# Kernel tuning notes

Hardware: AMD Instinct MI355X
Metric: run time of the kernel (lower is better)

The kernel has to match this reference:

```python
import jax, jax.numpy as jnp
import numpy as np

B, N, D = 8, 2048, 3
HIDDEN = (64, 128, 256)
LATENT = 128


def _layernorm(x, scale, bias, eps=1e-6):
    mu = jnp.mean(x, axis=-1, keepdims=True)
    var = jnp.mean((x - mu) ** 2, axis=-1, keepdims=True)
    return (x - mu) / jnp.sqrt(var + eps) * scale + bias


def setup_inputs() -> dict:
    key = jax.random.key(0)
    ks = jax.random.split(key, 8)
    inp = {
        "x": jax.random.normal(ks[0], (B, N, D), dtype=jnp.float32),
        "mask": jnp.ones((B, N), dtype=jnp.float32),
    }
    in_d = D
    for i, d in enumerate(HIDDEN):
        inp[f"W{i}"] = (jax.random.normal(ks[1 + i], (in_d, d), dtype=jnp.float32)
                        / np.float32(np.sqrt(in_d)))
        inp[f"b{i}"] = jnp.zeros((d,), dtype=jnp.float32)
        inp[f"g{i}"] = jnp.ones((d,), dtype=jnp.float32)
        inp[f"be{i}"] = jnp.zeros((d,), dtype=jnp.float32)
        in_d = d
    inp["Wz"] = (jax.random.normal(ks[5], (in_d, LATENT), dtype=jnp.float32)
                 / np.float32(np.sqrt(in_d)))
    inp["bz"] = jnp.zeros((LATENT,), dtype=jnp.float32)
    return inp


def reference(x, mask, W0, b0, g0, be0, W1, b1, g1, be1, W2, b2, g2, be2, Wz, bz):
    m = mask[..., None]                                   # (B, N, 1)
    count = jnp.sum(m, axis=1)                            # (B, 1)
    centroid = jnp.sum(x * m, axis=1, keepdims=True) / jnp.maximum(count, 1.0)[:, None, :]
    xc = x - centroid                                     # (B, N, D)

    # Pairwise squared distances; attention depends only on coordinates,
    # so it is identical for every layer -> compute once.
    diff = xc[:, :, None, :] - xc[:, None, :, :]          # (B, N, N, D)
    dist = jnp.sum(diff * diff, axis=-1)                  # (B, N, N)
    attn = jax.nn.softmax(-dist, axis=-1)                 # (B, N, N)

    h = xc
    for W, b, g, be in ((W0, b0, g0, be0), (W1, b1, g1, be1), (W2, b2, g2, be2)):
        h_agg = jnp.einsum('bij,bjd->bid', attn, h)       # weighted aggregation
        h = h_agg @ W + b
        h = _layernorm(h, g, be)
        h = jax.nn.swish(h)

    # Invariant readout: masked mean pool then Dense(latent)
    global_feat = jnp.sum(h * m, axis=1) / jnp.maximum(count, 1.0)
    z = global_feat @ Wz + bz                             # (B, latent)
    return z
```

## Files before the change

kernel.cpp:

```cpp
#include <hip/hip_runtime.h>
#include <hip/hip_bf16.h>

#define BATCH 8
#define NPTS 2048
#define LATENT 128

typedef __attribute__((ext_vector_type(8))) short short8;
typedef __attribute__((ext_vector_type(4))) float f32x4;

__device__ __forceinline__ ushort f2bf(float f) {
  unsigned int b = __float_as_uint(f);
  b += 0x7FFF + ((b >> 16) & 1);
  return (ushort)(b >> 16);
}
__device__ __forceinline__ float bf2f(ushort u) {
  return __uint_as_float(((unsigned int)u) << 16);
}
__device__ __forceinline__ unsigned int pkbf(float a, float b) {
  __hip_bfloat162 h = __float22bfloat162_rn(make_float2(a, b));
  return *(unsigned int*)&h;
}

typedef unsigned int __attribute__((address_space(1))) gas_uint;
typedef unsigned int __attribute__((address_space(3))) las_uint;
__device__ __forceinline__ void gl_lds16(const void* g, void* l) {
  __builtin_amdgcn_global_load_lds((const gas_uint*)g, (las_uint*)l, 16, 0, 0);
}

#define L2E 1.4426950408889634f
#define SC2 1.6986436f

__device__ __forceinline__ void wtrans_tile(const float* __restrict__ W,
    ushort* __restrict__ WT, int K, int N, int n0, int k0, int tid) {
  __shared__ ushort s[64][72];
  for (int i = tid; i < 64 * 64; i += 256) {
    const int kl = i >> 6, nl = i & 63;
    s[kl][nl] = f2bf(W[(size_t)(k0 + kl) * N + n0 + nl]);
  }
  __syncthreads();
  for (int i = tid; i < 64 * 64; i += 256) {
    const int nl = i >> 6, kl = i & 63;
    WT[(size_t)(n0 + nl) * K + k0 + kl] = s[kl][nl];
  }
}

__global__ __launch_bounds__(256) void setup_kernel(const float* __restrict__ x,
    const float* __restrict__ mask, float4* __restrict__ pnt,
    const float* __restrict__ W1, ushort* __restrict__ WT1,
    const float* __restrict__ W2, ushort* __restrict__ WT2,
    const float* __restrict__ Wz, ushort* __restrict__ WzT) {
  const int bid = blockIdx.x;
  const int tid = threadIdx.x;
  if (bid >= 8) {
    if (bid < 10) wtrans_tile(W1, WT1, 64, 128, (bid - 8) * 64, 0, tid);
    else if (bid < 18) {
      const int idx = bid - 10;
      wtrans_tile(W2, WT2, 128, 256, (idx & 3) * 64, (idx >> 2) * 64, tid);
    } else {
      const int idx = bid - 18;
      wtrans_tile(Wz, WzT, 256, 128, (idx & 1) * 64, (idx >> 1) * 64, tid);
    }
    return;
  }
  const int b = bid;
  const float* xb = x + (size_t)b * NPTS * 3;
  const float* mb = mask + (size_t)b * NPTS;
  float s0 = 0.f, s1 = 0.f, s2 = 0.f, c = 0.f;
  for (int n = tid; n < NPTS; n += 256) {
    float m = mb[n];
    s0 += xb[n * 3 + 0] * m;
    s1 += xb[n * 3 + 1] * m;
    s2 += xb[n * 3 + 2] * m;
    c += m;
  }
  __shared__ float red[4][256];
  red[0][tid] = s0; red[1][tid] = s1; red[2][tid] = s2; red[3][tid] = c;
  __syncthreads();
  for (int off = 128; off > 0; off >>= 1) {
    if (tid < off) {
      red[0][tid] += red[0][tid + off];
      red[1][tid] += red[1][tid + off];
      red[2][tid] += red[2][tid + off];
      red[3][tid] += red[3][tid + off];
    }
    __syncthreads();
  }
  const float cnt = fmaxf(red[3][0], 1.0f);
  const float c0 = red[0][0] / cnt, c1 = red[1][0] / cnt, c2 = red[2][0] / cnt;
  float4* pb = pnt + (size_t)b * NPTS;
  for (int n = tid; n < NPTS; n += 256) {
    const float a0 = xb[n * 3 + 0] - c0;
    const float a1 = xb[n * 3 + 1] - c1;
    const float a2 = xb[n * 3 + 2] - c2;
    pb[n] = make_float4(a0 * SC2, a1 * SC2, a2 * SC2,
                        -(a0 * a0 + a1 * a1 + a2 * a2) * L2E);
  }
}

__global__ __launch_bounds__(512) void layer0_kernel(
    const float4* __restrict__ pnt, const float* __restrict__ W,
    const float* __restrict__ bias, const float* __restrict__ g,
    const float* __restrict__ be, ushort* __restrict__ hout) {
  const int b = blockIdx.y;
  const int i0 = blockIdx.x * 64;
  const int tid = threadIdx.x;
  const int il = tid & 63, part = tid >> 6;
  const float4* pb = pnt + (size_t)b * NPTS;
  const float4 pi = pb[i0 + il];
  float a0 = 0.f, a1 = 0.f, a2 = 0.f, dn = 0.f;
#pragma unroll 8
  for (int j = part * 256; j < part * 256 + 256; j++) {
    const float4 pj = pb[j];
    float arg = pi.w + pj.w;
    arg = fmaf(pi.x, pj.x, arg);
    arg = fmaf(pi.y, pj.y, arg);
    arg = fmaf(pi.z, pj.z, arg);
    const float w = __builtin_amdgcn_exp2f(arg);
    a0 = fmaf(w, pj.x, a0);
    a1 = fmaf(w, pj.y, a1);
    a2 = fmaf(w, pj.z, a2);
    dn += w;
  }
  __shared__ float4 sred[8][64];
  __shared__ float srow[64 * 3];
  __shared__ ushort lt[64][64];
  sred[part][il] = make_float4(a0, a1, a2, dn);
  __syncthreads();
  if (tid < 64) {
    float A0 = 0.f, A1 = 0.f, A2 = 0.f, DN = 0.f;
#pragma unroll
    for (int p = 0; p < 8; p++) {
      const float4 r = sred[p][tid];
      A0 += r.x; A1 += r.y; A2 += r.z; DN += r.w;
    }
    const float inv = 1.0f / (DN * SC2);
    srow[tid * 3 + 0] = A0 * inv;
    srow[tid * 3 + 1] = A1 * inv;
    srow[tid * 3 + 2] = A2 * inv;
  }
  __syncthreads();
  const int wv = tid >> 6, lane = tid & 63;
  const float w0c = W[lane], w1c = W[64 + lane], w2c = W[128 + lane];
  const float gv = g[lane], bev = be[lane], bv = bias[lane];
#pragma unroll
  for (int r = 0; r < 8; r++) {
    const int row = wv * 8 + r;
    float o = bv;
    o = fmaf(srow[row * 3 + 0], w0c, o);
    o = fmaf(srow[row * 3 + 1], w1c, o);
    o = fmaf(srow[row * 3 + 2], w2c, o);
    float m1 = o, m2 = o * o;
#pragma unroll
    for (int off = 32; off > 0; off >>= 1) {
      m1 += __shfl_xor(m1, off, 64);
      m2 += __shfl_xor(m2, off, 64);
    }
    const float mu = m1 / 64.f;
    const float rstd = rsqrtf(m2 / 64.f - mu * mu + 1e-6f);
    const float v = (o - mu) * rstd * gv + bev;
    const float act = v / (1.0f + __expf(-v));
    lt[row][lane] = f2bf(act);
  }
  __syncthreads();
  if (tid < 64) {
    ushort tmp[64];
#pragma unroll
    for (int r = 0; r < 64; r++) tmp[r] = lt[r][tid];
    ushort* dst = hout + ((size_t)b * 64 + tid) * NPTS + i0;
#pragma unroll
    for (int c = 0; c < 8; c++)
      *(uint4*)(dst + c * 8) = *(uint4*)&tmp[c * 8];
  }
}

template <int DIN, int DOUT, bool POOL>
__global__ __launch_bounds__(512, 2) void fused_v5(
    const float4* __restrict__ pnt, const ushort* __restrict__ hT,
    const ushort* __restrict__ WT, const float* __restrict__ bias,
    const float* __restrict__ g, const float* __restrict__ be,
    ushort* __restrict__ hout, const float* __restrict__ mask,
    float* __restrict__ partial) {
  constexpr int NT = DIN / 16;
  constexpr int HALF = NPTS / 2;
  constexpr int TILES = HALF / 64;
  constexpr int NCOL = DOUT / 32;
  constexpr int PS = DIN + 8;
  constexpr int PN = DIN + 4;
  constexpr int SHT_B = 2 * 2 * DIN * 64 * 2;
  constexpr int SPNT_B = 2 * 2 * 64 * 16;
  constexpr int LOOP_B = SHT_B + SPNT_B;
  constexpr int SNUM_B = 64 * PN * 4;
  constexpr int OFF_SROW = SNUM_B;
  constexpr int OFF_SDEN = OFF_SROW + 64 * PS * 2;
  constexpr int OFF_SINV = OFF_SDEN + 256;
  constexpr int OFF_SSTAT = OFF_SINV + 256;
  constexpr int EPI_B = OFF_SSTAT + 1024;
  constexpr int SMEM_B = LOOP_B > EPI_B ? LOOP_B : EPI_B;
  __shared__ __align__(16) char smem[SMEM_B];
  ushort* sht = (ushort*)smem;
  float4* spnt = (float4*)(smem + SHT_B);

  const int b = blockIdx.y;
  const int i0 = blockIdx.x * 64;
  const int tid = threadIdx.x;
  const int wv = tid >> 6, lane = tid & 63;
  const int h = (wv >> 1) & 1;
  const int u = wv & 1;
  const int rg = wv >> 2;
  const int m = lane & 15, q = lane >> 4;
  const float4* pb = pnt + (size_t)b * NPTS;
  const ushort* hb = hT + (size_t)b * DIN * NPTS;

  const float4 pi0 = pb[i0 + rg * 32 + m];
  const float4 pi1 = pb[i0 + rg * 32 + 16 + m];

  f32x4 acc0[NT], acc1[NT];
#pragma unroll
  for (int nt = 0; nt < NT; nt++)
#pragma unroll
    for (int e = 0; e < 4; e++) { acc0[nt][e] = 0.f; acc1[nt][e] = 0.f; }
  float dacc0 = 0.f, dacc1 = 0.f;

  constexpr int NCH = DIN / 32;
  const int srow8 = lane >> 3;
  const int scsrc = (lane & 7) ^ srow8;
  const int jsw = ((lane & 7) << 3) | (lane >> 3);

  auto stage = [&](int t, int bf) {
    const int jb = t * 64;
#pragma unroll
    for (int i = 0; i < NCH; i++) {
      const int idx = wv * NCH + i;
      const int h2 = idx / (DIN / 8);
      const int oct = idx % (DIN / 8);
      const int row = oct * 8 + srow8;
      gl_lds16(hb + (size_t)row * NPTS + h2 * HALF + jb + scsrc * 8,
               sht + ((size_t)(bf * 2 + h2) * DIN + oct * 8) * 64);
    }
    if (wv == 0) {
#pragma unroll
      for (int h2 = 0; h2 < 2; h2++)
        gl_lds16(pb + h2 * HALF + jb + jsw, spnt + (bf * 2 + h2) * 64);
    }
  };

  stage(0, 0);
  __syncthreads();
  for (int t = 0; t < TILES; t++) {
    const int bf = t & 1;
    if (t + 1 < TILES) stage(t + 1, bf ^ 1);
    unsigned int au0[4], au1[4];
#pragma unroll
    for (int p = 0; p < 4; p++) {
      float wp[4];
#pragma unroll
      for (int e = 0; e < 2; e++) {
        const int jj = 2 * p + e;
        const float4 pj = spnt[(bf * 2 + h) * 64 + ((jj << 3) | (u * 4 + q))];
        float a0 = pi0.w + pj.w;
        a0 = fmaf(pi0.x, pj.x, a0);
        a0 = fmaf(pi0.y, pj.y, a0);
        a0 = fmaf(pi0.z, pj.z, a0);
        float a1 = pi1.w + pj.w;
        a1 = fmaf(pi1.x, pj.x, a1);
        a1 = fmaf(pi1.y, pj.y, a1);
        a1 = fmaf(pi1.z, pj.z, a1);
        wp[e] = __builtin_amdgcn_exp2f(a0);
        wp[2 + e] = __builtin_amdgcn_exp2f(a1);
      }
      dacc0 += wp[0] + wp[1];
      dacc1 += wp[2] + wp[3];
      au0[p] = pkbf(wp[0], wp[1]);
      au1[p] = pkbf(wp[2], wp[3]);
    }
    const short8 af0 = *(short8*)au0;
    const short8 af1 = *(short8*)au1;
#pragma unroll
    for (int nt = 0; nt < NT; nt++) {
      const int d = nt * 16 + m;
      const short8 bfr = *(const short8*)
          &sht[((size_t)(bf * 2 + h) * DIN + d) * 64 + (((u * 4 + q) ^ (m & 7)) << 3)];
      acc0[nt] = __builtin_amdgcn_mfma_f32_16x16x32_bf16(af0, bfr, acc0[nt], 0, 0, 0);
      acc1[nt] = __builtin_amdgcn_mfma_f32_16x16x32_bf16(af1, bfr, acc1[nt], 0, 0, 0);
    }
    __syncthreads();
  }

  float* snum = (float*)smem;
  ushort* srow = (ushort*)(smem + OFF_SROW);
  float* sden = (float*)(smem + OFF_SDEN);
  float* sinv = (float*)(smem + OFF_SINV);
  float* sstat = (float*)(smem + OFF_SSTAT);

  dacc0 += __shfl_xor(dacc0, 16, 64);
  dacc0 += __shfl_xor(dacc0, 32, 64);
  dacc1 += __shfl_xor(dacc1, 16, 64);
  dacc1 += __shfl_xor(dacc1, 32, 64);
  const int quarter = wv & 3;
  for (int p = 0; p < 4; p++) {
    if (quarter == p) {
      if (p == 0) {
#pragma unroll
        for (int nt = 0; nt < NT; nt++)
#pragma unroll
          for (int r = 0; r < 4; r++) {
            snum[(rg * 32 + q * 4 + r) * PN + nt * 16 + m] = acc0[nt][r];
            snum[(rg * 32 + 16 + q * 4 + r) * PN + nt * 16 + m] = acc1[nt][r];
          }
        if (q == 0) {
          sden[rg * 32 + m] = dacc0;
          sden[rg * 32 + 16 + m] = dacc1;
        }
      } else {
#pragma unroll
        for (int nt = 0; nt < NT; nt++)
#pragma unroll
          for (int r = 0; r < 4; r++) {
            snum[(rg * 32 + q * 4 + r) * PN + nt * 16 + m] += acc0[nt][r];
            snum[(rg * 32 + 16 + q * 4 + r) * PN + nt * 16 + m] += acc1[nt][r];
          }
        if (q == 0) {
          sden[rg * 32 + m] += dacc0;
          sden[rg * 32 + 16 + m] += dacc1;
        }
      }
    }
    __syncthreads();
  }
  if (tid < 64) sinv[tid] = 1.0f / sden[tid];
  __syncthreads();
  for (int idx = tid; idx < 64 * (DIN / 2); idx += 512) {
    const int r = idx / (DIN / 2), c2 = idx % (DIN / 2);
    const float v0 = snum[r * PN + 2 * c2] * sinv[r];
    const float v1 = snum[r * PN + 2 * c2 + 1] * sinv[r];
    *(unsigned int*)&srow[r * PS + 2 * c2] = pkbf(v0, v1);
  }
  __syncthreads();

  const int rg2 = wv >> 1, ch = wv & 1;
  short8 afrag[DIN / 32];
#pragma unroll
  for (int kt = 0; kt < DIN / 32; kt++)
    afrag[kt] = *(const short8*)&srow[(rg2 * 16 + m) * PS + kt * 32 + q * 8];
  f32x4 oacc[NCOL];
#pragma unroll
  for (int c = 0; c < NCOL; c++)
#pragma unroll
    for (int e = 0; e < 4; e++) oacc[c][e] = 0.f;
#pragma unroll
  for (int c = 0; c < NCOL; c++) {
    const int n0 = (ch * NCOL + c) * 16;
#pragma unroll
    for (int kt = 0; kt < DIN / 32; kt++) {
      const short8 bfrag = *(const short8*)(WT + (size_t)(n0 + m) * DIN + kt * 32 + q * 8);
      oacc[c] = __builtin_amdgcn_mfma_f32_16x16x32_bf16(afrag[kt], bfrag, oacc[c], 0, 0, 0);
    }
  }

  float bcol[NCOL];
#pragma unroll
  for (int c = 0; c < NCOL; c++) bcol[c] = bias[(ch * NCOL + c) * 16 + m];
#pragma unroll
  for (int r = 0; r < 4; r++) {
    float m1 = 0.f, m2 = 0.f;
#pragma unroll
    for (int c = 0; c < NCOL; c++) {
      const float v = oacc[c][r] + bcol[c];
      m1 += v; m2 += v * v;
    }
#pragma unroll
    for (int off = 8; off > 0; off >>= 1) {
      m1 += __shfl_xor(m1, off, 64);
      m2 += __shfl_xor(m2, off, 64);
    }
    if (m == 0) {
      const int row = rg2 * 16 + q * 4 + r;
      sstat[(row * 2 + ch) * 2 + 0] = m1;
      sstat[(row * 2 + ch) * 2 + 1] = m2;
    }
  }
  __syncthreads();

  ushort* lt = (ushort*)smem;
  float* spl = (float*)smem;
  float pacc[NCOL];
  if (POOL) {
#pragma unroll
    for (int c = 0; c < NCOL; c++) pacc[c] = 0.f;
  }
#pragma unroll
  for (int r = 0; r < 4; r++) {
    const int row = rg2 * 16 + q * 4 + r;
    const float m1 = sstat[(row * 2 + 0) * 2 + 0] + sstat[(row * 2 + 1) * 2 + 0];
    const float m2 = sstat[(row * 2 + 0) * 2 + 1] + sstat[(row * 2 + 1) * 2 + 1];
    const float mu = m1 / DOUT;
    const float rstd = rsqrtf(m2 / DOUT - mu * mu + 1e-6f);
    float mval = 0.f;
    if (POOL) mval = mask[(size_t)b * NPTS + i0 + row];
#pragma unroll
    for (int c = 0; c < NCOL; c++) {
      const int dco = (ch * NCOL + c) * 16 + m;
      const float v = (oacc[c][r] + bcol[c] - mu) * rstd * g[dco] + be[dco];
      const float act = v / (1.0f + __expf(-v));
      if (POOL) pacc[c] = fmaf(act, mval, pacc[c]);
      else lt[row * DOUT + dco] = f2bf(act);
    }
  }
  if (POOL) {
#pragma unroll
    for (int c = 0; c < NCOL; c++) {
      float v = pacc[c];
      v += __shfl_xor(v, 16, 64);
      v += __shfl_xor(v, 32, 64);
      if (q == 0) spl[rg2 * DOUT + (ch * NCOL + c) * 16 + m] = v;
    }
    __syncthreads();
    if (tid < DOUT)
      partial[((size_t)b * (NPTS / 64) + blockIdx.x) * DOUT + tid] =
          (spl[tid] + spl[DOUT + tid]) + (spl[2 * DOUT + tid] + spl[3 * DOUT + tid]);
  } else {
    __syncthreads();
    if (tid < DOUT) {
      ushort tmp[64];
#pragma unroll
      for (int r = 0; r < 64; r++) tmp[r] = lt[r * DOUT + tid];
      ushort* dst = hout + ((size_t)b * DOUT + tid) * NPTS + i0;
#pragma unroll
      for (int c = 0; c < 8; c++)
        *(uint4*)(dst + c * 8) = *(uint4*)&tmp[c * 8];
    }
  }
}

template <int DIN, int DOUT, bool POOL, int MINW>
__global__ __launch_bounds__(256, MINW) void fused_v6(
    const float4* __restrict__ pnt, const ushort* __restrict__ hT,
    const ushort* __restrict__ WT, const float* __restrict__ bias,
    const float* __restrict__ g, const float* __restrict__ be,
    ushort* __restrict__ hout, const float* __restrict__ mask,
    float* __restrict__ partial) {
  constexpr int NT = DIN / 16;
  constexpr int HALF = NPTS / 2;
  constexpr int TILES = HALF / 64;
  constexpr int NCOL = DOUT / 32;
  constexpr int PS = DIN + 8;
  constexpr int PN = DIN + 4;
  constexpr int SHT_B = 2 * 2 * DIN * 64 * 2;
  constexpr int SPNT_B = 2 * 2 * 64 * 16;
  constexpr int LOOP_B = SHT_B + SPNT_B;
  constexpr int SNUM_B = 32 * PN * 4;
  constexpr int OFF_SROW = SNUM_B;
  constexpr int OFF_SDEN = OFF_SROW + 32 * PS * 2;
  constexpr int OFF_SINV = OFF_SDEN + 128;
  constexpr int OFF_SSTAT = OFF_SINV + 128;
  constexpr int EPI_B = OFF_SSTAT + 512;
  constexpr int SMEM_B = LOOP_B > EPI_B ? LOOP_B : EPI_B;
  __shared__ __align__(16) char smem[SMEM_B];
  ushort* sht = (ushort*)smem;
  float4* spnt = (float4*)(smem + SHT_B);

  const int b = blockIdx.y;
  const int i0 = blockIdx.x * 32;
  const int tid = threadIdx.x;
  const int wv = tid >> 6, lane = tid & 63;
  const int h = wv >> 1;
  const int u = wv & 1;
  const int m = lane & 15, q = lane >> 4;
  const float4* pb = pnt + (size_t)b * NPTS;
  const ushort* hb = hT + (size_t)b * DIN * NPTS;

  const float4 pi0 = pb[i0 + m];
  const float4 pi1 = pb[i0 + 16 + m];

  f32x4 acc0[NT], acc1[NT];
#pragma unroll
  for (int nt = 0; nt < NT; nt++)
#pragma unroll
    for (int e = 0; e < 4; e++) { acc0[nt][e] = 0.f; acc1[nt][e] = 0.f; }
  float dacc0 = 0.f, dacc1 = 0.f;

  constexpr int NCH = DIN / 16;
  const int srow8 = lane >> 3;
  const int scsrc = (lane & 7) ^ srow8;
  const int jsw = ((lane & 7) << 3) | (lane >> 3);

  auto stage = [&](int t, int bf) {
    const int jb = t * 64;
#pragma unroll
    for (int i = 0; i < NCH; i++) {
      const int idx = wv * NCH + i;
      const int h2 = idx / (DIN / 8);
      const int oct = idx % (DIN / 8);
      const int row = oct * 8 + srow8;
      gl_lds16(hb + (size_t)row * NPTS + h2 * HALF + jb + scsrc * 8,
               sht + ((size_t)(bf * 2 + h2) * DIN + oct * 8) * 64);
    }
    if (wv == 0) {
#pragma unroll
      for (int h2 = 0; h2 < 2; h2++)
        gl_lds16(pb + h2 * HALF + jb + jsw, spnt + (bf * 2 + h2) * 64);
    }
  };

  stage(0, 0);
  __syncthreads();
  for (int t = 0; t < TILES; t++) {
    const int bf = t & 1;
    if (t + 1 < TILES) stage(t + 1, bf ^ 1);
    float w0a[8], w1a[8];
#pragma unroll
    for (int jj = 0; jj < 8; jj++) {
      const float4 pj = spnt[(bf * 2 + h) * 64 + ((jj << 3) | (u * 4 + q))];
      float a0 = pi0.w + pj.w;
      a0 = fmaf(pi0.x, pj.x, a0);
      a0 = fmaf(pi0.y, pj.y, a0);
      a0 = fmaf(pi0.z, pj.z, a0);
      float a1 = pi1.w + pj.w;
      a1 = fmaf(pi1.x, pj.x, a1);
      a1 = fmaf(pi1.y, pj.y, a1);
      a1 = fmaf(pi1.z, pj.z, a1);
      w0a[jj] = __builtin_amdgcn_exp2f(a0);
      w1a[jj] = __builtin_amdgcn_exp2f(a1);
      dacc0 += w0a[jj]; dacc1 += w1a[jj];
    }
    unsigned int au0[4], au1[4];
#pragma unroll
    for (int p = 0; p < 4; p++) {
      au0[p] = pkbf(w0a[2 * p], w0a[2 * p + 1]);
      au1[p] = pkbf(w1a[2 * p], w1a[2 * p + 1]);
    }
    const short8 af0 = *(short8*)au0;
    const short8 af1 = *(short8*)au1;
#pragma unroll
    for (int nt = 0; nt < NT; nt++) {
      const int d = nt * 16 + m;
      const short8 bfr = *(const short8*)
          &sht[((size_t)(bf * 2 + h) * DIN + d) * 64 + (((u * 4 + q) ^ (m & 7)) << 3)];
      acc0[nt] = __builtin_amdgcn_mfma_f32_16x16x32_bf16(af0, bfr, acc0[nt], 0, 0, 0);
      acc1[nt] = __builtin_amdgcn_mfma_f32_16x16x32_bf16(af1, bfr, acc1[nt], 0, 0, 0);
    }
    __syncthreads();
  }

  float* snum = (float*)smem;
  ushort* srow = (ushort*)(smem + OFF_SROW);
  float* sden = (float*)(smem + OFF_SDEN);
  float* sinv = (float*)(smem + OFF_SINV);
  float* sstat = (float*)(smem + OFF_SSTAT);

  dacc0 += __shfl_xor(dacc0, 16, 64);
  dacc0 += __shfl_xor(dacc0, 32, 64);
  dacc1 += __shfl_xor(dacc1, 16, 64);
  dacc1 += __shfl_xor(dacc1, 32, 64);
  for (int p = 0; p < 4; p++) {
    if (wv == p) {
      if (p == 0) {
#pragma unroll
        for (int nt = 0; nt < NT; nt++)
#pragma unroll
          for (int r = 0; r < 4; r++) {
            snum[(q * 4 + r) * PN + nt * 16 + m] = acc0[nt][r];
            snum[(16 + q * 4 + r) * PN + nt * 16 + m] = acc1[nt][r];
          }
        if (q == 0) { sden[m] = dacc0; sden[16 + m] = dacc1; }
      } else {
#pragma unroll
        for (int nt = 0; nt < NT; nt++)
#pragma unroll
          for (int r = 0; r < 4; r++) {
            snum[(q * 4 + r) * PN + nt * 16 + m] += acc0[nt][r];
            snum[(16 + q * 4 + r) * PN + nt * 16 + m] += acc1[nt][r];
          }
        if (q == 0) { sden[m] += dacc0; sden[16 + m] += dacc1; }
      }
    }
    __syncthreads();
  }
  if (tid < 32) sinv[tid] = 1.0f / sden[tid];
  __syncthreads();
  for (int idx = tid; idx < 32 * (DIN / 2); idx += 256) {
    const int r = idx / (DIN / 2), c2 = idx % (DIN / 2);
    const float v0 = snum[r * PN + 2 * c2] * sinv[r];
    const float v1 = snum[r * PN + 2 * c2 + 1] * sinv[r];
    *(unsigned int*)&srow[r * PS + 2 * c2] = pkbf(v0, v1);
  }
  __syncthreads();

  const int rg2 = wv >> 1, ch = wv & 1;
  short8 afrag[DIN / 32];
#pragma unroll
  for (int kt = 0; kt < DIN / 32; kt++)
    afrag[kt] = *(const short8*)&srow[(rg2 * 16 + m) * PS + kt * 32 + q * 8];
  f32x4 oacc[NCOL];
#pragma unroll
  for (int c = 0; c < NCOL; c++)
#pragma unroll
    for (int e = 0; e < 4; e++) oacc[c][e] = 0.f;
#pragma unroll
  for (int c = 0; c < NCOL; c++) {
    const int n0 = (ch * NCOL + c) * 16;
#pragma unroll
    for (int kt = 0; kt < DIN / 32; kt++) {
      const short8 bfrag = *(const short8*)(WT + (size_t)(n0 + m) * DIN + kt * 32 + q * 8);
      oacc[c] = __builtin_amdgcn_mfma_f32_16x16x32_bf16(afrag[kt], bfrag, oacc[c], 0, 0, 0);
    }
  }

  float bcol[NCOL];
#pragma unroll
  for (int c = 0; c < NCOL; c++) bcol[c] = bias[(ch * NCOL + c) * 16 + m];
#pragma unroll
  for (int r = 0; r < 4; r++) {
    float m1 = 0.f, m2 = 0.f;
#pragma unroll
    for (int c = 0; c < NCOL; c++) {
      const float v = oacc[c][r] + bcol[c];
      m1 += v; m2 += v * v;
    }
#pragma unroll
    for (int off = 8; off > 0; off >>= 1) {
      m1 += __shfl_xor(m1, off, 64);
      m2 += __shfl_xor(m2, off, 64);
    }
    if (m == 0) {
      const int row = rg2 * 16 + q * 4 + r;
      sstat[(row * 2 + ch) * 2 + 0] = m1;
      sstat[(row * 2 + ch) * 2 + 1] = m2;
    }
  }
  __syncthreads();

  ushort* lt = (ushort*)smem;
  float* spl = (float*)smem;
  float pacc[NCOL];
  if (POOL) {
#pragma unroll
    for (int c = 0; c < NCOL; c++) pacc[c] = 0.f;
  }
#pragma unroll
  for (int r = 0; r < 4; r++) {
    const int row = rg2 * 16 + q * 4 + r;
    const float m1 = sstat[(row * 2 + 0) * 2 + 0] + sstat[(row * 2 + 1) * 2 + 0];
    const float m2 = sstat[(row * 2 + 0) * 2 + 1] + sstat[(row * 2 + 1) * 2 + 1];
    const float mu = m1 / DOUT;
    const float rstd = rsqrtf(m2 / DOUT - mu * mu + 1e-6f);
    float mval = 0.f;
    if (POOL) mval = mask[(size_t)b * NPTS + i0 + row];
#pragma unroll
    for (int c = 0; c < NCOL; c++) {
      const int dco = (ch * NCOL + c) * 16 + m;
      const float v = (oacc[c][r] + bcol[c] - mu) * rstd * g[dco] + be[dco];
      const float act = v / (1.0f + __expf(-v));
      if (POOL) pacc[c] = fmaf(act, mval, pacc[c]);
      else lt[row * DOUT + dco] = f2bf(act);
    }
  }
  if (POOL) {
#pragma unroll
    for (int c = 0; c < NCOL; c++) {
      float v = pacc[c];
      v += __shfl_xor(v, 16, 64);
      v += __shfl_xor(v, 32, 64);
      if (q == 0) spl[rg2 * DOUT + (ch * NCOL + c) * 16 + m] = v;
    }
    __syncthreads();
    if (tid < DOUT)
      partial[((size_t)b * (NPTS / 32) + blockIdx.x) * DOUT + tid] =
          spl[tid] + spl[DOUT + tid];
  } else {
    __syncthreads();
    if (tid < DOUT) {
      ushort tmp[32];
#pragma unroll
      for (int r = 0; r < 32; r++) tmp[r] = lt[r * DOUT + tid];
      ushort* dst = hout + ((size_t)b * DOUT + tid) * NPTS + i0;
#pragma unroll
      for (int c = 0; c < 4; c++)
        *(uint4*)(dst + c * 8) = *(uint4*)&tmp[c * 8];
    }
  }
}

__global__ __launch_bounds__(256) void readout_kernel(
    const float* __restrict__ partial, const float* __restrict__ mask,
    const ushort* __restrict__ WzT, const float* __restrict__ bz,
    float* __restrict__ out) {
  const int b = blockIdx.x;
  const int tid = threadIdx.x;
  const float* pb = partial + (size_t)b * (NPTS / 64) * 256;
  float s0 = 0.f, s1 = 0.f, s2 = 0.f, s3 = 0.f;
#pragma unroll
  for (int p = 0; p < NPTS / 64; p += 4) {
    s0 += pb[(size_t)(p + 0) * 256 + tid];
    s1 += pb[(size_t)(p + 1) * 256 + tid];
    s2 += pb[(size_t)(p + 2) * 256 + tid];
    s3 += pb[(size_t)(p + 3) * 256 + tid];
  }
  const float s = (s0 + s1) + (s2 + s3);
  const float* mb = mask + (size_t)b * NPTS;
  float c = 0.f;
  for (int n = tid; n < NPTS; n += 256) c += mb[n];
  __shared__ float red[256];
  red[tid] = c;
  __syncthreads();
  for (int off = 128; off > 0; off >>= 1) {
    if (tid < off) red[tid] += red[tid + off];
    __syncthreads();
  }
  const float cnt = fmaxf(red[0], 1.0f);
  __shared__ float gf[256];
  gf[tid] = s / cnt;
  __syncthreads();
  const int col = tid & 127, part = tid >> 7;
  float z = 0.f;
  const ushort* wr = WzT + (size_t)col * 256 + part * 128;
  const float* gp = gf + part * 128;
#pragma unroll 4
  for (int d = 0; d < 128; d += 8) {
    const short8 w8 = *(const short8*)(wr + d);
#pragma unroll
    for (int e = 0; e < 8; e++)
      z = fmaf(gp[d + e], bf2f((ushort)w8[e]), z);
  }
  __shared__ float zred[256];
  zred[tid] = z;
  __syncthreads();
  if (tid < LATENT)
    out[(size_t)b * LATENT + tid] = bz[tid] + zred[tid] + zred[128 + tid];
}

extern "C" void kernel_launch(void* const* d_in, const int* in_sizes, int n_in,
                              void* d_out, int out_size, void* d_ws, size_t ws_size,
                              hipStream_t stream) {
  const float* x    = (const float*)d_in[0];
  const float* mask = (const float*)d_in[1];
  const float* W0   = (const float*)d_in[2];
  const float* b0   = (const float*)d_in[3];
  const float* g0   = (const float*)d_in[4];
  const float* be0  = (const float*)d_in[5];
  const float* W1   = (const float*)d_in[6];
  const float* b1   = (const float*)d_in[7];
  const float* g1   = (const float*)d_in[8];
  const float* be1  = (const float*)d_in[9];
  const float* W2   = (const float*)d_in[10];
  const float* b2   = (const float*)d_in[11];
  const float* g2   = (const float*)d_in[12];
  const float* be2  = (const float*)d_in[13];
  const float* Wz   = (const float*)d_in[14];
  const float* bz   = (const float*)d_in[15];
  float* out = (float*)d_out;

  char* ws = (char*)d_ws;
  float4* pnt     = (float4*)(ws);
  ushort* h1T     = (ushort*)(ws + 262144);
  ushort* h2T     = (ushort*)(ws + 2359296);
  float*  partial = (float*)(ws + 6553600);
  ushort* WT1     = (ushort*)(ws + 6815744);
  ushort* WT2     = (ushort*)(ws + 6832128);
  ushort* WzT     = (ushort*)(ws + 6897664);

  setup_kernel<<<dim3(26), dim3(256), 0, stream>>>(
      x, mask, pnt, W1, WT1, W2, WT2, Wz, WzT);

  layer0_kernel<<<dim3(NPTS / 64, BATCH), dim3(512), 0, stream>>>(
      pnt, W0, b0, g0, be0, h1T);

  fused_v6<64, 128, false, 4><<<dim3(NPTS / 32, BATCH), dim3(256), 0, stream>>>(
      pnt, h1T, WT1, b1, g1, be1, h2T, nullptr, nullptr);

  fused_v5<128, 256, true><<<dim3(NPTS / 64, BATCH), dim3(512), 0, stream>>>(
      pnt, h2T, WT2, b2, g2, be2, nullptr, mask, partial);

  readout_kernel<<<dim3(BATCH), dim3(256), 0, stream>>>(partial, mask, WzT, bz, out);
}
```

Measured before the change: 183.3 us.

## Precompute bf16 attention weights once and reuse across layer GEMMs

Adds a kernel that computes the unnormalized exp attention weights once, stores them as bf16 in a global buffer (64 MB total) and accumulates per-row partial sums and denominators. The layer-1 and layer-2 GEMM kernels then load these precomputed A fragments instead of recomputing distances and exp2 per tile, and read the denominators from the partial buffer. Layer 0 becomes a small MLP kernel that reduces the partials. This removes repeated transcendental work across three layers at the cost of heavy global memory traffic for writing and twice reading the weight matrix.

```diff
diff --git a/kernel.cpp b/kernel.cpp
--- a/kernel.cpp
+++ b/kernel.cpp
@@ -97,89 +97,125 @@
   }
 }
 
-__global__ __launch_bounds__(512) void layer0_kernel(
-    const float4* __restrict__ pnt, const float* __restrict__ W,
+__global__ __launch_bounds__(128) void wgen_kernel(
+    const float4* __restrict__ pnt, ushort* __restrict__ Wt,
+    float4* __restrict__ part) {
+  const int js = blockIdx.x;
+  const int it = blockIdx.y;
+  const int b = blockIdx.z;
+  const int tid = threadIdx.x;
+  const int i = it * 128 + tid;
+  const float4* pb = pnt + (size_t)b * NPTS;
+  const float4 pi = pb[i];
+  float a0 = 0.f, a1 = 0.f, a2 = 0.f, dn = 0.f;
+  ushort* wb = Wt + (size_t)b * 256 * NPTS * 8;
+  for (int jt = js * 32; jt < js * 32 + 32; jt++) {
+    unsigned int au[4];
+#pragma unroll
+    for (int e2 = 0; e2 < 4; e2++) {
+      float wv0, wv1;
+      {
+        const float4 pj = pb[jt * 8 + e2 * 2 + 0];
+        float arg = pi.w + pj.w;
+        arg = fmaf(pi.x, pj.x, arg);
+        arg = fmaf(pi.y, pj.y, arg);
+        arg = fmaf(pi.z, pj.z, arg);
+        wv0 = __builtin_amdgcn_exp2f(arg);
+        dn += wv0;
+        a0 = fmaf(wv0, pj.x, a0);
+        a1 = fmaf(wv0, pj.y, a1);
+        a2 = fmaf(wv0, pj.z, a2);
+      }
+      {
+        const float4 pj = pb[jt * 8 + e2 * 2 + 1];
+        float arg = pi.w + pj.w;
+        arg = fmaf(pi.x, pj.x, arg);
+        arg = fmaf(pi.y, pj.y, arg);
+        arg = fmaf(pi.z, pj.z, arg);
+        wv1 = __builtin_amdgcn_exp2f(arg);
+        dn += wv1;
+        a0 = fmaf(wv1, pj.x, a0);
+        a1 = fmaf(wv1, pj.y, a1);
+        a2 = fmaf(wv1, pj.z, a2);
+      }
+      au[e2] = pkbf(wv0, wv1);
+    }
+    *(uint4*)(wb + ((size_t)jt * NPTS + i) * 8) = *(uint4*)au;
+  }
+  part[(size_t)js * (BATCH * NPTS) + (size_t)b * NPTS + i] =
+      make_float4(a0, a1, a2, dn);
+}
+
+__global__ __launch_bounds__(256) void mlp0_kernel(
+    const float4* __restrict__ part, const float* __restrict__ W,
     const float* __restrict__ bias, const float* __restrict__ g,
     const float* __restrict__ be, ushort* __restrict__ hout) {
-  const int b = blockIdx.y;
-  const int i0 = blockIdx.x * 64;
+  constexpr int DIN = 3, DOUT = 64;
   const int tid = threadIdx.x;
-  const int il = tid & 63, part = tid >> 6;
-  const float4* pb = pnt + (size_t)b * NPTS;
-  const float4 pi = pb[i0 + il];
-  float a0 = 0.f, a1 = 0.f, a2 = 0.f, dn = 0.f;
-#pragma unroll 8
-  for (int j = part * 256; j < part * 256 + 256; j++) {
-    const float4 pj = pb[j];
-    float arg = pi.w + pj.w;
-    arg = fmaf(pi.x, pj.x, arg);
-    arg = fmaf(pi.y, pj.y, arg);
-    arg = fmaf(pi.z, pj.z, arg);
-    const float w = __builtin_amdgcn_exp2f(arg);
-    a0 = fmaf(w, pj.x, a0);
-    a1 = fmaf(w, pj.y, a1);
-    a2 = fmaf(w, pj.z, a2);
-    dn += w;
-  }
-  __shared__ float4 sred[8][64];
-  __shared__ float srow[64 * 3];
-  __shared__ ushort lt[64][64];
-  sred[part][il] = make_float4(a0, a1, a2, dn);
-  __syncthreads();
-  if (tid < 64) {
-    float A0 = 0.f, A1 = 0.f, A2 = 0.f, DN = 0.f;
-#pragma unroll
-    for (int p = 0; p < 8; p++) {
-      const float4 r = sred[p][tid];
-      A0 += r.x; A1 += r.y; A2 += r.z; DN += r.w;
-    }
-    const float inv = 1.0f / (DN * SC2);
-    srow[tid * 3 + 0] = A0 * inv;
-    srow[tid * 3 + 1] = A1 * inv;
-    srow[tid * 3 + 2] = A2 * inv;
-  }
-  __syncthreads();
   const int wv = tid >> 6, lane = tid & 63;
-  const float w0c = W[lane], w1c = W[64 + lane], w2c = W[128 + lane];
-  const float gv = g[lane], bev = be[lane], bv = bias[lane];
-#pragma unroll
-  for (int r = 0; r < 8; r++) {
-    const int row = wv * 8 + r;
-    float o = bv;
-    o = fmaf(srow[row * 3 + 0], w0c, o);
-    o = fmaf(srow[row * 3 + 1], w1c, o);
-    o = fmaf(srow[row * 3 + 2], w2c, o);
-    float m1 = o, m2 = o * o;
+  const int r0 = blockIdx.x * 16;
+  const int bb = r0 / NPTS;
+  const int nn = r0 % NPTS;
+  __shared__ float srow[16 * DIN];
+  if (tid < 16) {
+    float4 s = part[(size_t)bb * NPTS + nn + tid];
+#pragma unroll
+    for (int p = 1; p < 8; p++) {
+      const float4 t = part[(size_t)p * (BATCH * NPTS) + (size_t)bb * NPTS + nn + tid];
+      s.x += t.x; s.y += t.y; s.z += t.z; s.w += t.w;
+    }
+    const float inv = 1.0f / (s.w * SC2);
+    srow[tid * 3 + 0] = s.x * inv;
+    srow[tid * 3 + 1] = s.y * inv;
+    srow[tid * 3 + 2] = s.z * inv;
+  }
+  __syncthreads();
+
+  float o[4];
+  const float bv = bias[lane];
+#pragma unroll
+  for (int r = 0; r < 4; r++) o[r] = bv;
+#pragma unroll
+  for (int k = 0; k < DIN; k++) {
+    const float wk = W[(size_t)k * DOUT + lane];
+#pragma unroll
+    for (int r = 0; r < 4; r++)
+      o[r] = fmaf(srow[(wv * 4 + r) * DIN + k], wk, o[r]);
+  }
+  __shared__ ushort lt[16][DOUT];
+#pragma unroll
+  for (int r = 0; r < 4; r++) {
+    float m1 = o[r], m2 = o[r] * o[r];
 #pragma unroll
     for (int off = 32; off > 0; off >>= 1) {
       m1 += __shfl_xor(m1, off, 64);
       m2 += __shfl_xor(m2, off, 64);
     }
-    const float mu = m1 / 64.f;
-    const float rstd = rsqrtf(m2 / 64.f - mu * mu + 1e-6f);
-    const float v = (o - mu) * rstd * gv + bev;
+    const float mu = m1 / DOUT;
+    const float var = m2 / DOUT - mu * mu;
+    const float rstd = rsqrtf(var + 1e-6f);
+    const float v = (o[r] - mu) * rstd * g[lane] + be[lane];
     const float act = v / (1.0f + __expf(-v));
-    lt[row][lane] = f2bf(act);
-  }
-  __syncthreads();
-  if (tid < 64) {
-    ushort tmp[64];
-#pragma unroll
-    for (int r = 0; r < 64; r++) tmp[r] = lt[r][tid];
-    ushort* dst = hout + ((size_t)b * 64 + tid) * NPTS + i0;
-#pragma unroll
-    for (int c = 0; c < 8; c++)
-      *(uint4*)(dst + c * 8) = *(uint4*)&tmp[c * 8];
+    lt[wv * 4 + r][lane] = f2bf(act);
+  }
+  __syncthreads();
+  if (tid < DOUT) {
+    ushort tmp[16];
+#pragma unroll
+    for (int r = 0; r < 16; r++) tmp[r] = lt[r][tid];
+    ushort* dst = hout + ((size_t)bb * DOUT + tid) * NPTS + nn;
+    *(uint4*)dst = *(uint4*)&tmp[0];
+    *(uint4*)(dst + 8) = *(uint4*)&tmp[8];
   }
 }
 
 template <int DIN, int DOUT, bool POOL>
-__global__ __launch_bounds__(512, 2) void fused_v5(
-    const float4* __restrict__ pnt, const ushort* __restrict__ hT,
-    const ushort* __restrict__ WT, const float* __restrict__ bias,
-    const float* __restrict__ g, const float* __restrict__ be,
-    ushort* __restrict__ hout, const float* __restrict__ mask,
-    float* __restrict__ partial) {
+__global__ __launch_bounds__(512, 2) void gemm_v5(
+    const ushort* __restrict__ Wt, const float4* __restrict__ part,
+    const ushort* __restrict__ hT, const ushort* __restrict__ WT,
+    const float* __restrict__ bias, const float* __restrict__ g,
+    const float* __restrict__ be, ushort* __restrict__ hout,
+    const float* __restrict__ mask, float* __restrict__ partial) {
   constexpr int NT = DIN / 16;
   constexpr int HALF = NPTS / 2;
   constexpr int TILES = HALF / 64;
@@ -187,18 +223,15 @@
   constexpr int PS = DIN + 8;
   constexpr int PN = DIN + 4;
   constexpr int SHT_B = 2 * 2 * DIN * 64 * 2;
-  constexpr int SPNT_B = 2 * 2 * 64 * 16;
-  constexpr int LOOP_B = SHT_B + SPNT_B;
+  constexpr int LOOP_B = SHT_B;
   constexpr int SNUM_B = 64 * PN * 4;
   constexpr int OFF_SROW = SNUM_B;
-  constexpr int OFF_SDEN = OFF_SROW + 64 * PS * 2;
-  constexpr int OFF_SINV = OFF_SDEN + 256;
+  constexpr int OFF_SINV = OFF_SROW + 64 * PS * 2;
   constexpr int OFF_SSTAT = OFF_SINV + 256;
   constexpr int EPI_B = OFF_SSTAT + 1024;
   constexpr int SMEM_B = LOOP_B > EPI_B ? LOOP_B : EPI_B;
   __shared__ __align__(16) char smem[SMEM_B];
   ushort* sht = (ushort*)smem;
-  float4* spnt = (float4*)(smem + SHT_B);
 
   const int b = blockIdx.y;
   const int i0 = blockIdx.x * 64;
@@ -208,23 +241,21 @@
   const int u = wv & 1;
   const int rg = wv >> 2;
   const int m = lane & 15, q = lane >> 4;
-  const float4* pb = pnt + (size_t)b * NPTS;
   const ushort* hb = hT + (size_t)b * DIN * NPTS;
-
-  const float4 pi0 = pb[i0 + rg * 32 + m];
-  const float4 pi1 = pb[i0 + rg * 32 + 16 + m];
+  const ushort* wtb = Wt + (size_t)b * 256 * NPTS * 8;
+
+  const ushort* arow0 = wtb + ((size_t)(h * 128 + u * 4 + q) * NPTS + i0 + rg * 32 + m) * 8;
+  const ushort* arow1 = arow0 + 16 * 8;
 
   f32x4 acc0[NT], acc1[NT];
 #pragma unroll
   for (int nt = 0; nt < NT; nt++)
 #pragma unroll
     for (int e = 0; e < 4; e++) { acc0[nt][e] = 0.f; acc1[nt][e] = 0.f; }
-  float dacc0 = 0.f, dacc1 = 0.f;
 
   constexpr int NCH = DIN / 32;
   const int srow8 = lane >> 3;
   const int scsrc = (lane & 7) ^ srow8;
-  const int jsw = ((lane & 7) << 3) | (lane >> 3);
 
   auto stage = [&](int t, int bf) {
     const int jb = t * 64;
@@ -237,11 +268,6 @@
       gl_lds16(hb + (size_t)row * NPTS + h2 * HALF + jb + scsrc * 8,
                sht + ((size_t)(bf * 2 + h2) * DIN + oct * 8) * 64);
     }
-    if (wv == 0) {
-#pragma unroll
-      for (int h2 = 0; h2 < 2; h2++)
-        gl_lds16(pb + h2 * HALF + jb + jsw, spnt + (bf * 2 + h2) * 64);
-    }
   };
 
   stage(0, 0);
@@ -249,32 +275,8 @@
   for (int t = 0; t < TILES; t++) {
     const int bf = t & 1;
     if (t + 1 < TILES) stage(t + 1, bf ^ 1);
-    unsigned int au0[4], au1[4];
-#pragma unroll
-    for (int p = 0; p < 4; p++) {
-      float wp[4];
-#pragma unroll
-      for (int e = 0; e < 2; e++) {
-        const int jj = 2 * p + e;
-        const float4 pj = spnt[(bf * 2 + h) * 64 + ((jj << 3) | (u * 4 + q))];
-        float a0 = pi0.w + pj.w;
-        a0 = fmaf(pi0.x, pj.x, a0);
-        a0 = fmaf(pi0.y, pj.y, a0);
-        a0 = fmaf(pi0.z, pj.z, a0);
-        float a1 = pi1.w + pj.w;
-        a1 = fmaf(pi1.x, pj.x, a1);
-        a1 = fmaf(pi1.y, pj.y, a1);
-        a1 = fmaf(pi1.z, pj.z, a1);
-        wp[e] = __builtin_amdgcn_exp2f(a0);
-        wp[2 + e] = __builtin_amdgcn_exp2f(a1);
-      }
-      dacc0 += wp[0] + wp[1];
-      dacc1 += wp[2] + wp[3];
-      au0[p] = pkbf(wp[0], wp[1]);
-      au1[p] = pkbf(wp[2], wp[3]);
-    }
-    const short8 af0 = *(short8*)au0;
-    const short8 af1 = *(short8*)au1;
+    const short8 af0 = *(const short8*)(arow0 + (size_t)t * 8 * NPTS * 8);
+    const short8 af1 = *(const short8*)(arow1 + (size_t)t * 8 * NPTS * 8);
 #pragma unroll
     for (int nt = 0; nt < NT; nt++) {
       const int d = nt * 16 + m;
@@ -288,14 +290,9 @@
 
   float* snum = (float*)smem;
   ushort* srow = (ushort*)(smem + OFF_SROW);
-  float* sden = (float*)(smem + OFF_SDEN);
   float* sinv = (float*)(smem + OFF_SINV);
   float* sstat = (float*)(smem + OFF_SSTAT);
 
-  dacc0 += __shfl_xor(dacc0, 16, 64);
-  dacc0 += __shfl_xor(dacc0, 32, 64);
-  dacc1 += __shfl_xor(dacc1, 16, 64);
-  dacc1 += __shfl_xor(dacc1, 32, 64);
   const int quarter = wv & 3;
   for (int p = 0; p < 4; p++) {
     if (quarter == p) {
@@ -307,10 +304,6 @@
             snum[(rg * 32 + q * 4 + r) * PN + nt * 16 + m] = acc0[nt][r];
             snum[(rg * 32 + 16 + q * 4 + r) * PN + nt * 16 + m] = acc1[nt][r];
           }
-        if (q == 0) {
-          sden[rg * 32 + m] = dacc0;
-          sden[rg * 32 + 16 + m] = dacc1;
-        }
       } else {
 #pragma unroll
         for (int nt = 0; nt < NT; nt++)
@@ -319,15 +312,17 @@
             snum[(rg * 32 + q * 4 + r) * PN + nt * 16 + m] += acc0[nt][r];
             snum[(rg * 32 + 16 + q * 4 + r) * PN + nt * 16 + m] += acc1[nt][r];
           }
-        if (q == 0) {
-          sden[rg * 32 + m] += dacc0;
-          sden[rg * 32 + 16 + m] += dacc1;
-        }
       }
     }
     __syncthreads();
   }
-  if (tid < 64) sinv[tid] = 1.0f / sden[tid];
+  if (tid < 64) {
+    float d = part[(size_t)b * NPTS + i0 + tid].w;
+#pragma unroll
+    for (int p = 1; p < 8; p++)
+      d += part[(size_t)p * (BATCH * NPTS) + (size_t)b * NPTS + i0 + tid].w;
+    sinv[tid] = 1.0f / d;
+  }
   __syncthreads();
   for (int idx = tid; idx < 64 * (DIN / 2); idx += 512) {
     const int r = idx / (DIN / 2), c2 = idx % (DIN / 2);
@@ -433,12 +428,12 @@
 }
 
 template <int DIN, int DOUT, bool POOL, int MINW>
-__global__ __launch_bounds__(256, MINW) void fused_v6(
-    const float4* __restrict__ pnt, const ushort* __restrict__ hT,
-    const ushort* __restrict__ WT, const float* __restrict__ bias,
-    const float* __restrict__ g, const float* __restrict__ be,
-    ushort* __restrict__ hout, const float* __restrict__ mask,
-    float* __restrict__ partial) {
+__global__ __launch_bounds__(256, MINW) void gemm_v6(
+    const ushort* __restrict__ Wt, const float4* __restrict__ part,
+    const ushort* __restrict__ hT, const ushort* __restrict__ WT,
+    const float* __restrict__ bias, const float* __restrict__ g,
+    const float* __restrict__ be, ushort* __restrict__ hout,
+    const float* __restrict__ mask, float* __restrict__ partial) {
   constexpr int NT = DIN / 16;
   constexpr int HALF = NPTS / 2;
   constexpr int TILES = HALF / 64;
@@ -446,18 +441,15 @@
   constexpr int PS = DIN + 8;
   constexpr int PN = DIN + 4;
   constexpr int SHT_B = 2 * 2 * DIN * 64 * 2;
-  constexpr int SPNT_B = 2 * 2 * 64 * 16;
-  constexpr int LOOP_B = SHT_B + SPNT_B;
+  constexpr int LOOP_B = SHT_B;
   constexpr int SNUM_B = 32 * PN * 4;
   constexpr int OFF_SROW = SNUM_B;
-  constexpr int OFF_SDEN = OFF_SROW + 32 * PS * 2;
-  constexpr int OFF_SINV = OFF_SDEN + 128;
+  constexpr int OFF_SINV = OFF_SROW + 32 * PS * 2;
   constexpr int OFF_SSTAT = OFF_SINV + 128;
   constexpr int EPI_B = OFF_SSTAT + 512;
   constexpr int SMEM_B = LOOP_B > EPI_B ? LOOP_B : EPI_B;
   __shared__ __align__(16) char smem[SMEM_B];
   ushort* sht = (ushort*)smem;
-  float4* spnt = (float4*)(smem + SHT_B);
 
   const int b = blockIdx.y;
   const int i0 = blockIdx.x * 32;
@@ -466,23 +458,21 @@
   const int h = wv >> 1;
   const int u = wv & 1;
   const int m = lane & 15, q = lane >> 4;
-  const float4* pb = pnt + (size_t)b * NPTS;
   const ushort* hb = hT + (size_t)b * DIN * NPTS;
-
-  const float4 pi0 = pb[i0 + m];
-  const float4 pi1 = pb[i0 + 16 + m];
+  const ushort* wtb = Wt + (size_t)b * 256 * NPTS * 8;
+
+  const ushort* arow0 = wtb + ((size_t)(h * 128 + u * 4 + q) * NPTS + i0 + m) * 8;
+  const ushort* arow1 = arow0 + 16 * 8;
 
   f32x4 acc0[NT], acc1[NT];
 #pragma unroll
   for (int nt = 0; nt < NT; nt++)
 #pragma unroll
     for (int e = 0; e < 4; e++) { acc0[nt][e] = 0.f; acc1[nt][e] = 0.f; }
-  float dacc0 = 0.f, dacc1 = 0.f;
 
   constexpr int NCH = DIN / 16;
   const int srow8 = lane >> 3;
   const int scsrc = (lane & 7) ^ srow8;
-  const int jsw = ((lane & 7) << 3) | (lane >> 3);
 
   auto stage = [&](int t, int bf) {
     const int jb = t * 64;
@@ -495,11 +485,6 @@
       gl_lds16(hb + (size_t)row * NPTS + h2 * HALF + jb + scsrc * 8,
                sht + ((size_t)(bf * 2 + h2) * DIN + oct * 8) * 64);
     }
-    if (wv == 0) {
-#pragma unroll
-      for (int h2 = 0; h2 < 2; h2++)
-        gl_lds16(pb + h2 * HALF + jb + jsw, spnt + (bf * 2 + h2) * 64);
-    }
   };
 
   stage(0, 0);
@@ -507,30 +492,8 @@
   for (int t = 0; t < TILES; t++) {
     const int bf = t & 1;
     if (t + 1 < TILES) stage(t + 1, bf ^ 1);
-    float w0a[8], w1a[8];
-#pragma unroll
-    for (int jj = 0; jj < 8; jj++) {
-      const float4 pj = spnt[(bf * 2 + h) * 64 + ((jj << 3) | (u * 4 + q))];
-      float a0 = pi0.w + pj.w;
-      a0 = fmaf(pi0.x, pj.x, a0);
-      a0 = fmaf(pi0.y, pj.y, a0);
-      a0 = fmaf(pi0.z, pj.z, a0);
-      float a1 = pi1.w + pj.w;
-      a1 = fmaf(pi1.x, pj.x, a1);
-      a1 = fmaf(pi1.y, pj.y, a1);
-      a1 = fmaf(pi1.z, pj.z, a1);
-      w0a[jj] = __builtin_amdgcn_exp2f(a0);
-      w1a[jj] = __builtin_amdgcn_exp2f(a1);
-      dacc0 += w0a[jj]; dacc1 += w1a[jj];
-    }
-    unsigned int au0[4], au1[4];
-#pragma unroll
-    for (int p = 0; p < 4; p++) {
-      au0[p] = pkbf(w0a[2 * p], w0a[2 * p + 1]);
-      au1[p] = pkbf(w1a[2 * p], w1a[2 * p + 1]);
-    }
-    const short8 af0 = *(short8*)au0;
-    const short8 af1 = *(short8*)au1;
+    const short8 af0 = *(const short8*)(arow0 + (size_t)t * 8 * NPTS * 8);
+    const short8 af1 = *(const short8*)(arow1 + (size_t)t * 8 * NPTS * 8);
 #pragma unroll
     for (int nt = 0; nt < NT; nt++) {
       const int d = nt * 16 + m;
@@ -544,14 +507,9 @@
 
   float* snum = (float*)smem;
   ushort* srow = (ushort*)(smem + OFF_SROW);
-  float* sden = (float*)(smem + OFF_SDEN);
   float* sinv = (float*)(smem + OFF_SINV);
   float* sstat = (float*)(smem + OFF_SSTAT);
 
-  dacc0 += __shfl_xor(dacc0, 16, 64);
-  dacc0 += __shfl_xor(dacc0, 32, 64);
-  dacc1 += __shfl_xor(dacc1, 16, 64);
-  dacc1 += __shfl_xor(dacc1, 32, 64);
   for (int p = 0; p < 4; p++) {
     if (wv == p) {
       if (p == 0) {
@@ -562,7 +520,6 @@
             snum[(q * 4 + r) * PN + nt * 16 + m] = acc0[nt][r];
             snum[(16 + q * 4 + r) * PN + nt * 16 + m] = acc1[nt][r];
           }
-        if (q == 0) { sden[m] = dacc0; sden[16 + m] = dacc1; }
       } else {
 #pragma unroll
         for (int nt = 0; nt < NT; nt++)
@@ -571,12 +528,17 @@
             snum[(q * 4 + r) * PN + nt * 16 + m] += acc0[nt][r];
             snum[(16 + q * 4 + r) * PN + nt * 16 + m] += acc1[nt][r];
           }
-        if (q == 0) { sden[m] += dacc0; sden[16 + m] += dacc1; }
       }
     }
     __syncthreads();
   }
-  if (tid < 32) sinv[tid] = 1.0f / sden[tid];
+  if (tid < 32) {
+    float d = part[(size_t)b * NPTS + i0 + tid].w;
+#pragma unroll
+    for (int p = 1; p < 8; p++)
+      d += part[(size_t)p * (BATCH * NPTS) + (size_t)b * NPTS + i0 + tid].w;
+    sinv[tid] = 1.0f / d;
+  }
   __syncthreads();
   for (int idx = tid; idx < 32 * (DIN / 2); idx += 256) {
     const int r = idx / (DIN / 2), c2 = idx % (DIN / 2);
@@ -758,18 +720,22 @@
   ushort* WT1     = (ushort*)(ws + 6815744);
   ushort* WT2     = (ushort*)(ws + 6832128);
   ushort* WzT     = (ushort*)(ws + 6897664);
+  float4* part    = (float4*)(ws + 6963200);
+  ushort* Wt      = (ushort*)(ws + 9060352);
 
   setup_kernel<<<dim3(26), dim3(256), 0, stream>>>(
       x, mask, pnt, W1, WT1, W2, WT2, Wz, WzT);
 
-  layer0_kernel<<<dim3(NPTS / 64, BATCH), dim3(512), 0, stream>>>(
-      pnt, W0, b0, g0, be0, h1T);
-
-  fused_v6<64, 128, false, 4><<<dim3(NPTS / 32, BATCH), dim3(256), 0, stream>>>(
-      pnt, h1T, WT1, b1, g1, be1, h2T, nullptr, nullptr);
-
-  fused_v5<128, 256, true><<<dim3(NPTS / 64, BATCH), dim3(512), 0, stream>>>(
-      pnt, h2T, WT2, b2, g2, be2, nullptr, mask, partial);
+  wgen_kernel<<<dim3(8, 16, BATCH), dim3(128), 0, stream>>>(pnt, Wt, part);
+
+  mlp0_kernel<<<dim3(BATCH * NPTS / 16), dim3(256), 0, stream>>>(
+      part, W0, b0, g0, be0, h1T);
+
+  gemm_v6<64, 128, false, 4><<<dim3(NPTS / 32, BATCH), dim3(256), 0, stream>>>(
+      Wt, part, h1T, WT1, b1, g1, be1, h2T, nullptr, nullptr);
+
+  gemm_v5<128, 256, true><<<dim3(NPTS / 64, BATCH), dim3(512), 0, stream>>>(
+      Wt, part, h2T, WT2, b2, g2, be2, nullptr, mask, partial);
 
   readout_kernel<<<dim3(BATCH), dim3(256), 0, stream>>>(partial, mask, WzT, bz, out);
 }
```

Measured after the change: 179.1 us. -2.3%, faster.
